# Performance work log

Measured on AMD Instinct MI355X. Metric: run time of the kernel, lower is better.

The kernel has to match this reference:

```python
import jax, jax.numpy as jnp
import numpy as np

N_NODES = 50000
N_EDGES = 800000
D = 128


def setup_inputs() -> dict:
    key = jax.random.key(0)
    k1, k2, k3, k4, k5 = jax.random.split(key, 5)
    feature = jax.random.normal(k1, (N_NODES, D), dtype=jnp.float32)
    src = jax.random.randint(k2, (N_EDGES,), 0, N_NODES, dtype=jnp.int64)
    dst = jax.random.randint(k3, (N_EDGES,), 0, N_NODES, dtype=jnp.int64)
    # Linear(in_feats=128, out_feats=128) params
    W = jax.random.normal(k4, (D, D), dtype=jnp.float32) * (1.0 / np.sqrt(D))
    b = jax.random.normal(k5, (D,), dtype=jnp.float32) * 0.01
    return {"feature": feature, "src": src, "dst": dst, "W": W, "b": b}


def reference(feature, src, dst, W, b):
    n = feature.shape[0]
    # copy_src message: each edge carries h[src]; segment-mean over in-edges at dst
    msgs = feature[src]                                      # [E, D] irregular gather
    summed = jax.ops.segment_sum(msgs, dst, num_segments=n)  # [N, D] scatter-add
    cnt = jax.ops.segment_sum(jnp.ones((src.shape[0],), dtype=feature.dtype),
                              dst, num_segments=n)           # in-degree per node
    h = summed / jnp.clip(cnt, 1.0)[:, None]                 # mean (isolated nodes -> 0)
    # NodeApplyModule: ReLU(W h + b)
    return jax.nn.relu(h @ W.T + b)
```

## Files before the change

### kernel.cpp

```cpp
#include <hip/hip_runtime.h>

#define NN 50000
#define NE 800000
#define DD 128
#define NPAD 50176
#define NSB 49
#define GB 784
#define HB 782


#define ACC4(A, V) { A.x += V.x; A.y += V.y; A.z += V.z; A.w += V.w; }

#define BSUM_PREFIX(bsum, sbase)                                   \
  {                                                                \
    int tt = threadIdx.x;                                          \
    if (tt < 64) {                                                 \
      int b = (tt < NSB) ? bsum[tt] : 0;                           \
      int z = b;                                                   \
      _Pragma("unroll") for (int o = 1; o < 64; o <<= 1) {         \
        int w_ = __shfl_up(z, o);                                  \
        if (tt >= o) z += w_;                                      \
      }                                                            \
      sbase[tt] = z - b;                                           \
    }                                                              \
    __syncthreads();                                               \
  }

__global__ __launch_bounds__(128) void k_gemm_hist(
    const float* __restrict__ feat, const float* __restrict__ W,
    float* __restrict__ g, const int* __restrict__ dst, int* __restrict__ cnt) {
  __shared__ float fs[32][132];
  __shared__ float ws[32][68];
  int tid = threadIdx.x;
  int bid = blockIdx.x;

  if (bid >= GB) {
    int idx = (bid - GB) * 128 + tid;
    if (idx < NE / 8) {
      const int4* d4 = (const int4*)dst;
      int4 a = d4[idx * 2];
      int4 b = d4[idx * 2 + 1];
      atomicAdd(&cnt[a.x], 1); atomicAdd(&cnt[a.y], 1);
      atomicAdd(&cnt[a.z], 1); atomicAdd(&cnt[a.w], 1);
      atomicAdd(&cnt[b.x], 1); atomicAdd(&cnt[b.y], 1);
      atomicAdd(&cnt[b.z], 1); atomicAdd(&cnt[b.w], 1);
    }
    return;
  }

  int row0 = (bid >> 1) * 128;
  int col0 = (bid & 1) * 64;
  int tc = tid & 7;
  int trb = tid >> 3;
  int wbase = tc * 8 + ((tc >> 2) << 2);
  float acc[8][8] = {};

  for (int kc = 0; kc < 4; ++kc) {
    if (kc) __syncthreads();
    for (int i = 0; i < 8; ++i) {
      int fidx = tid + (i << 7);
      int r = fidx >> 3, q = fidx & 7;
      int grow = row0 + r;
      float4 v = make_float4(0.f, 0.f, 0.f, 0.f);
      if (grow < NN) v = ((const float4*)feat)[grow * 32 + kc * 8 + q];
      int k = q << 2;
      fs[k][r] = v.x; fs[k + 1][r] = v.y; fs[k + 2][r] = v.z; fs[k + 3][r] = v.w;
    }
    for (int i = 0; i < 4; ++i) {
      int fidx = tid + (i << 7);
      int c = fidx >> 3, q = fidx & 7;
      float4 v = ((const float4*)W)[(col0 + c) * 32 + kc * 8 + q];
      int sc = c + ((c >> 5) << 2);
      int k = q << 2;
      ws[k][sc] = v.x; ws[k + 1][sc] = v.y; ws[k + 2][sc] = v.z; ws[k + 3][sc] = v.w;
    }
    __syncthreads();

#define FM8(R, H)                                                       \
    { acc[R][0] += (H)*w0.x; acc[R][1] += (H)*w0.y;                     \
      acc[R][2] += (H)*w0.z; acc[R][3] += (H)*w0.w;                     \
      acc[R][4] += (H)*w1.x; acc[R][5] += (H)*w1.y;                     \
      acc[R][6] += (H)*w1.z; acc[R][7] += (H)*w1.w; }

#pragma unroll 8
    for (int k = 0; k < 32; ++k) {
      float4 w0 = *(const float4*)&ws[k][wbase];
      float4 w1 = *(const float4*)&ws[k][wbase + 4];
      float4 h0 = *(const float4*)&fs[k][trb * 8];
      float4 h1 = *(const float4*)&fs[k][trb * 8 + 4];
      FM8(0, h0.x) FM8(1, h0.y) FM8(2, h0.z) FM8(3, h0.w)
      FM8(4, h1.x) FM8(5, h1.y) FM8(6, h1.z) FM8(7, h1.w)
    }
  }

#pragma unroll
  for (int r = 0; r < 8; ++r) {
    int grow = row0 + trb * 8 + r;
    if (grow < NN) {
      float4 o0, o1;
      o0.x = acc[r][0]; o0.y = acc[r][1]; o0.z = acc[r][2]; o0.w = acc[r][3];
      o1.x = acc[r][4]; o1.y = acc[r][5]; o1.z = acc[r][6]; o1.w = acc[r][7];
      float4* gp = (float4*)(g + (size_t)grow * DD + col0) + tc * 2;
      gp[0] = o0;
      gp[1] = o1;
    }
  }
}

__global__ __launch_bounds__(1024) void k_scan(const int* __restrict__ cnt,
                                               int* __restrict__ pos,
                                               int* __restrict__ bsum) {
  __shared__ int wsum[16];
  int t = threadIdx.x;
  int gidx = blockIdx.x * 1024 + t;
  int v = cnt[gidx];
  int x = v;
#pragma unroll
  for (int o = 1; o < 64; o <<= 1) {
    int y = __shfl_up(x, o);
    if ((t & 63) >= o) x += y;
  }
  if ((t & 63) == 63) wsum[t >> 6] = x;
  __syncthreads();
  if (t < 64) {
    int y = (t < 16) ? wsum[t] : 0;
    int z = y;
#pragma unroll
    for (int o = 1; o < 16; o <<= 1) {
      int w = __shfl_up(z, o);
      if (t >= o) z += w;
    }
    if (t < 16) wsum[t] = z - y;
  }
  __syncthreads();
  pos[gidx] = wsum[t >> 6] + x - v;
  if (t == 1023) bsum[blockIdx.x] = wsum[15] + x;
}

__global__ __launch_bounds__(256) void k_fill(const int* __restrict__ src,
                                              const int* __restrict__ dst,
                                              int* __restrict__ pos,
                                              int* __restrict__ csr,
                                              const int* __restrict__ bsum) {
  __shared__ int sbase[64];
  BSUM_PREFIX(bsum, sbase)
  int idx = blockIdx.x * 256 + threadIdx.x;
  if (idx < NE / 4) {
    int4 d = ((const int4*)dst)[idx];
    int4 s = ((const int4*)src)[idx];
    int p;
    p = atomicAdd(&pos[d.x], 1); csr[sbase[d.x >> 10] + p] = s.x;
    p = atomicAdd(&pos[d.y], 1); csr[sbase[d.y >> 10] + p] = s.y;
    p = atomicAdd(&pos[d.z], 1); csr[sbase[d.z >> 10] + p] = s.z;
    p = atomicAdd(&pos[d.w], 1); csr[sbase[d.w >> 10] + p] = s.w;
  }
}

__global__ __launch_bounds__(256) void k_gmean(const float* __restrict__ g,
                                               const int* __restrict__ csr,
                                               const int* __restrict__ pos,
                                               const int* __restrict__ cnt,
                                               const int* __restrict__ bsum,
                                               const float* __restrict__ bias,
                                               float* __restrict__ out) {
  __shared__ int sbase[64];
  BSUM_PREFIX(bsum, sbase)
  int tid = threadIdx.x;
  int hw = tid >> 5, l32 = tid & 31;
  int n = blockIdx.x * 8 + hw;
  int c = cnt[n];
  int endg = sbase[n >> 10] + pos[n];
  int start = endg - c;
  float4 a0 = make_float4(0.f, 0.f, 0.f, 0.f), a1 = a0, a2 = a0, a3 = a0;

  for (int base = start; base < endg; base += 32) {
    int m = endg - base;
    if (m > 32) m = 32;
    int s = (l32 < m) ? csr[base + l32] : 0;
    int j = 0;
    for (; j + 8 <= m; j += 8) {
      int s0 = __shfl(s, j + 0, 32), s1 = __shfl(s, j + 1, 32),
          s2 = __shfl(s, j + 2, 32), s3 = __shfl(s, j + 3, 32),
          s4 = __shfl(s, j + 4, 32), s5 = __shfl(s, j + 5, 32),
          s6 = __shfl(s, j + 6, 32), s7 = __shfl(s, j + 7, 32);
      float4 v0 = ((const float4*)(g + (size_t)s0 * DD))[l32];
      float4 v1 = ((const float4*)(g + (size_t)s1 * DD))[l32];
      float4 v2 = ((const float4*)(g + (size_t)s2 * DD))[l32];
      float4 v3 = ((const float4*)(g + (size_t)s3 * DD))[l32];
      float4 v4 = ((const float4*)(g + (size_t)s4 * DD))[l32];
      float4 v5 = ((const float4*)(g + (size_t)s5 * DD))[l32];
      float4 v6 = ((const float4*)(g + (size_t)s6 * DD))[l32];
      float4 v7 = ((const float4*)(g + (size_t)s7 * DD))[l32];
      ACC4(a0, v0) ACC4(a1, v1) ACC4(a2, v2) ACC4(a3, v3)
      ACC4(a0, v4) ACC4(a1, v5) ACC4(a2, v6) ACC4(a3, v7)
    }
    for (; j < m; ++j) {
      int sj = __shfl(s, j, 32);
      float4 v = ((const float4*)(g + (size_t)sj * DD))[l32];
      ACC4(a0, v)
    }
  }
  a0.x += a1.x + a2.x + a3.x;
  a0.y += a1.y + a2.y + a3.y;
  a0.z += a1.z + a2.z + a3.z;
  a0.w += a1.w + a2.w + a3.w;
  float inv = 1.0f / fmaxf((float)c, 1.0f);
  float4 b4 = ((const float4*)bias)[l32];
  float4 o;
  o.x = fmaxf(a0.x * inv + b4.x, 0.f);
  o.y = fmaxf(a0.y * inv + b4.y, 0.f);
  o.z = fmaxf(a0.z * inv + b4.z, 0.f);
  o.w = fmaxf(a0.w * inv + b4.w, 0.f);
  ((float4*)(out + (size_t)n * DD))[l32] = o;
}

__global__ __launch_bounds__(128) void k_hist(const int* __restrict__ dst,
                                              int* __restrict__ cnt) {
  int idx = blockIdx.x * 128 + threadIdx.x;
  if (idx < NE / 8) {
    const int4* d4 = (const int4*)dst;
    int4 a = d4[idx * 2];
    int4 b = d4[idx * 2 + 1];
    atomicAdd(&cnt[a.x], 1); atomicAdd(&cnt[a.y], 1);
    atomicAdd(&cnt[a.z], 1); atomicAdd(&cnt[a.w], 1);
    atomicAdd(&cnt[b.x], 1); atomicAdd(&cnt[b.y], 1);
    atomicAdd(&cnt[b.z], 1); atomicAdd(&cnt[b.w], 1);
  }
}

__global__ __launch_bounds__(256) void k_gsum(const float* __restrict__ feat,
                                              const int* __restrict__ csr,
                                              const int* __restrict__ pos,
                                              const int* __restrict__ cnt,
                                              const int* __restrict__ bsum,
                                              float* __restrict__ out) {
  __shared__ int sbase[64];
  BSUM_PREFIX(bsum, sbase)
  int tid = threadIdx.x;
  int hw = tid >> 5, l32 = tid & 31;
  int n = blockIdx.x * 8 + hw;
  int c = cnt[n];
  int endg = sbase[n >> 10] + pos[n];
  int start = endg - c;
  float4 a0 = make_float4(0.f, 0.f, 0.f, 0.f), a1 = a0;
  for (int base = start; base < endg; base += 32) {
    int m = endg - base;
    if (m > 32) m = 32;
    int s = (l32 < m) ? csr[base + l32] : 0;
    for (int j = 0; j < m; ++j) {
      int sj = __shfl(s, j, 32);
      float4 v = ((const float4*)(feat + (size_t)sj * DD))[l32];
      if (j & 1) { ACC4(a1, v) } else { ACC4(a0, v) }
    }
  }
  a0.x += a1.x; a0.y += a1.y; a0.z += a1.z; a0.w += a1.w;
  ((float4*)(out + (size_t)n * DD))[l32] = a0;
}

__global__ __launch_bounds__(256) void k_gemm_inplace(float* __restrict__ io,
                                                      const int* __restrict__ cnt,
                                                      const float* __restrict__ W,
                                                      const float* __restrict__ bias) {
  __shared__ float Wt[64][132];
  __shared__ __attribute__((aligned(16))) float hs[64][72];
  int tid = threadIdx.x;
  int row0 = blockIdx.x * 64;
  int tc = tid & 31;
  int tr = tid >> 5;
  float acc[8][4] = {};
  for (int p = 0; p < 2; ++p) {
    if (p) __syncthreads();
    for (int i = 0; i < 8; ++i) {
      int fidx = tid + (i << 8);
      int c = fidx >> 4;
      int kq = fidx & 15;
      float4 w = ((const float4*)W)[c * 32 + p * 16 + kq];
      int kk = kq << 2;
      Wt[kk + 0][c ^ (((kk + 0) & 31) << 2)] = w.x;
      Wt[kk + 1][c ^ (((kk + 1) & 31) << 2)] = w.y;
      Wt[kk + 2][c ^ (((kk + 2) & 31) << 2)] = w.z;
      Wt[kk + 3][c ^ (((kk + 3) & 31) << 2)] = w.w;
    }
    for (int i = 0; i < 4; ++i) {
      int fidx = tid + (i << 8);
      int r = fidx & 63;
      int kq = fidx >> 6;
      int grow = row0 + r;
      float4 v = make_float4(0.f, 0.f, 0.f, 0.f);
      if (grow < NN) {
        v = ((const float4*)io)[(size_t)grow * 32 + p * 16 + kq];
        float inv = 1.0f / fmaxf((float)cnt[grow], 1.0f);
        v.x *= inv; v.y *= inv; v.z *= inv; v.w *= inv;
      }
      int kk = kq << 2;
      hs[kk + 0][r] = v.x;
      hs[kk + 1][r] = v.y;
      hs[kk + 2][r] = v.z;
      hs[kk + 3][r] = v.w;
    }
    __syncthreads();
#pragma unroll 4
    for (int kk = 0; kk < 64; ++kk) {
      float4 w4 = *(const float4*)&Wt[kk][(tc << 2) ^ ((kk & 31) << 2)];
      float4 h0 = *(const float4*)&hs[kk][tr << 3];
      float4 h1 = *(const float4*)&hs[kk][(tr << 3) + 4];
      acc[0][0] += h0.x * w4.x; acc[0][1] += h0.x * w4.y; acc[0][2] += h0.x * w4.z; acc[0][3] += h0.x * w4.w;
      acc[1][0] += h0.y * w4.x; acc[1][1] += h0.y * w4.y; acc[1][2] += h0.y * w4.z; acc[1][3] += h0.y * w4.w;
      acc[2][0] += h0.z * w4.x; acc[2][1] += h0.z * w4.y; acc[2][2] += h0.z * w4.z; acc[2][3] += h0.z * w4.w;
      acc[3][0] += h0.w * w4.x; acc[3][1] += h0.w * w4.y; acc[3][2] += h0.w * w4.z; acc[3][3] += h0.w * w4.w;
      acc[4][0] += h1.x * w4.x; acc[4][1] += h1.x * w4.y; acc[4][2] += h1.x * w4.z; acc[4][3] += h1.x * w4.w;
      acc[5][0] += h1.y * w4.x; acc[5][1] += h1.y * w4.y; acc[5][2] += h1.y * w4.z; acc[5][3] += h1.y * w4.w;
      acc[6][0] += h1.z * w4.x; acc[6][1] += h1.z * w4.y; acc[6][2] += h1.z * w4.z; acc[6][3] += h1.z * w4.w;
      acc[7][0] += h1.w * w4.x; acc[7][1] += h1.w * w4.y; acc[7][2] += h1.w * w4.z; acc[7][3] += h1.w * w4.w;
    }
  }
  float4 b4 = ((const float4*)bias)[tc];
#pragma unroll
  for (int r = 0; r < 8; ++r) {
    int row = row0 + (tr << 3) + r;
    if (row < NN) {
      float4 o;
      o.x = fmaxf(acc[r][0] + b4.x, 0.f);
      o.y = fmaxf(acc[r][1] + b4.y, 0.f);
      o.z = fmaxf(acc[r][2] + b4.z, 0.f);
      o.w = fmaxf(acc[r][3] + b4.w, 0.f);
      ((float4*)(io + (size_t)row * DD))[tc] = o;
    }
  }
}

extern "C" void kernel_launch(void* const* d_in, const int* in_sizes, int n_in,
                              void* d_out, int out_size, void* d_ws, size_t ws_size,
                              hipStream_t stream) {
  const float* feature = (const float*)d_in[0];
  const int*   src     = (const int*)d_in[1];
  const int*   dst     = (const int*)d_in[2];
  const float* W       = (const float*)d_in[3];
  const float* bias    = (const float*)d_in[4];
  float* out = (float*)d_out;

  int* cnt  = (int*)d_ws;
  int* pos  = cnt + NPAD;
  int* bsum = pos + NPAD;
  int* csr  = bsum + 64;
  float* g  = (float*)(csr + NE);

  size_t need_main = (size_t)(2 * NPAD + 64 + NE) * 4 + (size_t)NN * DD * 4;

  hipMemsetAsync(cnt, 0, NPAD * sizeof(int), stream);

  if (ws_size >= need_main) {
    hipLaunchKernelGGL(k_gemm_hist, dim3(GB + HB), dim3(128), 0, stream,
                       feature, W, g, dst, cnt);
    hipLaunchKernelGGL(k_scan, dim3(NSB), dim3(1024), 0, stream, cnt, pos, bsum);
    hipLaunchKernelGGL(k_fill, dim3((NE / 4 + 255) / 256), dim3(256), 0, stream,
                       src, dst, pos, csr, bsum);
    hipLaunchKernelGGL(k_gmean, dim3(NN / 8), dim3(256), 0, stream,
                       g, csr, pos, cnt, bsum, bias, out);
  } else {
    hipLaunchKernelGGL(k_hist, dim3(HB), dim3(128), 0, stream, dst, cnt);
    hipLaunchKernelGGL(k_scan, dim3(NSB), dim3(1024), 0, stream, cnt, pos, bsum);
    hipLaunchKernelGGL(k_fill, dim3((NE / 4 + 255) / 256), dim3(256), 0, stream,
                       src, dst, pos, csr, bsum);
    hipLaunchKernelGGL(k_gsum, dim3(NN / 8), dim3(256), 0, stream,
                       feature, csr, pos, cnt, bsum, out);
    hipLaunchKernelGGL(k_gemm_inplace, dim3((NN + 63) / 64), dim3(256), 0,
                       stream, out, cnt, W, bias);
  }
}
```

Before: 252.0 us.

## Restructure feature GEMM to keep full W resident in LDS with persistent wavefronts

The tiled 128x64 GEMM with chunked K staging is replaced by a persistent-block scheme. Each 256-thread block loads the whole 128x128 W into shared memory once, using an XOR swizzle against bank conflicts, then each wavefront loops over 8-row groups of features, computing two output columns per lane. This is meant to cut repeated W reloads and per-chunk syncs, and the histogram blocks are resized to 256 threads. In exchange, each lane has far less register reuse per shared-memory read (8x2 outputs), and 80KB of LDS per block limits occupancy.

```diff
diff --git a/kernel.cpp b/kernel.cpp
--- a/kernel.cpp
+++ b/kernel.cpp
@@ -5,7 +5,8 @@
 #define DD 128
 #define NPAD 50176
 #define NSB 49
-#define GB 784
+#define WGB 512
+#define HBW 391
 #define HB 782
 
 
@@ -26,16 +27,16 @@
     __syncthreads();                                               \
   }
 
-__global__ __launch_bounds__(128) void k_gemm_hist(
+__global__ __launch_bounds__(256) void k_gemm_hist(
     const float* __restrict__ feat, const float* __restrict__ W,
     float* __restrict__ g, const int* __restrict__ dst, int* __restrict__ cnt) {
-  __shared__ float fs[32][132];
-  __shared__ float ws[32][68];
+  __shared__ float4 Wc4[DD * 32];
+  __shared__ float hs[4][8][DD];
   int tid = threadIdx.x;
   int bid = blockIdx.x;
 
-  if (bid >= GB) {
-    int idx = (bid - GB) * 128 + tid;
+  if (bid >= WGB) {
+    int idx = (bid - WGB) * 256 + tid;
     if (idx < NE / 8) {
       const int4* d4 = (const int4*)dst;
       int4 a = d4[idx * 2];
@@ -48,61 +49,47 @@
     return;
   }
 
-  int row0 = (bid >> 1) * 128;
-  int col0 = (bid & 1) * 64;
-  int tc = tid & 7;
-  int trb = tid >> 3;
-  int wbase = tc * 8 + ((tc >> 2) << 2);
-  float acc[8][8] = {};
-
-  for (int kc = 0; kc < 4; ++kc) {
-    if (kc) __syncthreads();
-    for (int i = 0; i < 8; ++i) {
-      int fidx = tid + (i << 7);
-      int r = fidx >> 3, q = fidx & 7;
-      int grow = row0 + r;
-      float4 v = make_float4(0.f, 0.f, 0.f, 0.f);
-      if (grow < NN) v = ((const float4*)feat)[grow * 32 + kc * 8 + q];
-      int k = q << 2;
-      fs[k][r] = v.x; fs[k + 1][r] = v.y; fs[k + 2][r] = v.z; fs[k + 3][r] = v.w;
-    }
-    for (int i = 0; i < 4; ++i) {
-      int fidx = tid + (i << 7);
-      int c = fidx >> 3, q = fidx & 7;
-      float4 v = ((const float4*)W)[(col0 + c) * 32 + kc * 8 + q];
-      int sc = c + ((c >> 5) << 2);
-      int k = q << 2;
-      ws[k][sc] = v.x; ws[k + 1][sc] = v.y; ws[k + 2][sc] = v.z; ws[k + 3][sc] = v.w;
-    }
-    __syncthreads();
-
-#define FM8(R, H)                                                       \
-    { acc[R][0] += (H)*w0.x; acc[R][1] += (H)*w0.y;                     \
-      acc[R][2] += (H)*w0.z; acc[R][3] += (H)*w0.w;                     \
-      acc[R][4] += (H)*w1.x; acc[R][5] += (H)*w1.y;                     \
-      acc[R][6] += (H)*w1.z; acc[R][7] += (H)*w1.w; }
-
-#pragma unroll 8
-    for (int k = 0; k < 32; ++k) {
-      float4 w0 = *(const float4*)&ws[k][wbase];
-      float4 w1 = *(const float4*)&ws[k][wbase + 4];
-      float4 h0 = *(const float4*)&fs[k][trb * 8];
-      float4 h1 = *(const float4*)&fs[k][trb * 8 + 4];
-      FM8(0, h0.x) FM8(1, h0.y) FM8(2, h0.z) FM8(3, h0.w)
-      FM8(4, h1.x) FM8(5, h1.y) FM8(6, h1.z) FM8(7, h1.w)
-    }
-  }
-
-#pragma unroll
-  for (int r = 0; r < 8; ++r) {
-    int grow = row0 + trb * 8 + r;
-    if (grow < NN) {
-      float4 o0, o1;
-      o0.x = acc[r][0]; o0.y = acc[r][1]; o0.z = acc[r][2]; o0.w = acc[r][3];
-      o1.x = acc[r][4]; o1.y = acc[r][5]; o1.z = acc[r][6]; o1.w = acc[r][7];
-      float4* gp = (float4*)(g + (size_t)grow * DD + col0) + tc * 2;
-      gp[0] = o0;
-      gp[1] = o1;
+  {
+    const float4* W4 = (const float4*)W;
+#pragma unroll
+    for (int i = 0; i < 16; ++i) {
+      int fidx = tid + (i << 8);
+      int c = fidx >> 5, kq = fidx & 31;
+      Wc4[c * 32 + (kq ^ (c & 31))] = W4[fidx];
+    }
+  }
+  __syncthreads();
+
+  int w = tid >> 6, lane = tid & 63;
+  int s = lane & 31;
+  const float2* feat2 = (const float2*)feat;
+
+  for (int gid = bid * 4 + w; gid < NN / 8; gid += WGB * 4) {
+    int r0 = gid * 8;
+#pragma unroll
+    for (int r = 0; r < 8; ++r) {
+      float2 v = feat2[(size_t)(r0 + r) * 64 + lane];
+      hs[w][r][lane * 2] = v.x;
+      hs[w][r][lane * 2 + 1] = v.y;
+    }
+    float2 acc[8] = {};
+#pragma unroll 2
+    for (int kc = 0; kc < 32; ++kc) {
+      float4 w0 = Wc4[lane * 32 + (kc ^ s)];
+      float4 w1 = Wc4[(lane + 64) * 32 + (kc ^ s)];
+#pragma unroll
+      for (int r = 0; r < 8; ++r) {
+        float4 h = *(const float4*)&hs[w][r][kc * 4];
+        acc[r].x += h.x * w0.x; acc[r].x += h.y * w0.y;
+        acc[r].x += h.z * w0.z; acc[r].x += h.w * w0.w;
+        acc[r].y += h.x * w1.x; acc[r].y += h.y * w1.y;
+        acc[r].y += h.z * w1.z; acc[r].y += h.w * w1.w;
+      }
+    }
+#pragma unroll
+    for (int r = 0; r < 8; ++r) {
+      g[(size_t)(r0 + r) * DD + lane] = acc[r].x;
+      g[(size_t)(r0 + r) * DD + lane + 64] = acc[r].y;
     }
   }
 }
@@ -350,7 +337,7 @@
   hipMemsetAsync(cnt, 0, NPAD * sizeof(int), stream);
 
   if (ws_size >= need_main) {
-    hipLaunchKernelGGL(k_gemm_hist, dim3(GB + HB), dim3(128), 0, stream,
+    hipLaunchKernelGGL(k_gemm_hist, dim3(WGB + HBW), dim3(256), 0, stream,
                        feature, W, g, dst, cnt);
     hipLaunchKernelGGL(k_scan, dim3(NSB), dim3(1024), 0, stream, cnt, pos, bsum);
     hipLaunchKernelGGL(k_fill, dim3((NE / 4 + 255) / 256), dim3(256), 0, stream,
```

Result: faster. 240.3 us (-4.6%).
